# Kernel tuning notes

Measured on AMD Instinct MI355X. Metric: run time of the kernel, lower is better.

## Reference

```python
import jax, jax.numpy as jnp
import numpy as np

N, E, CIN, A, C, NB, B = 20000, 100000, 64, 32, 256, 4, 128
FD = C * NB  # fusion_dims = channels + c_growth*(n_blocks_out-1) with c_growth==channels
HID = 1024


def setup_inputs() -> dict:
    key = jax.random.key(0)
    ks = jax.random.split(key, 24)
    s = 0.05
    inp = {
        "x": jax.random.normal(ks[0], (N, CIN), jnp.float32),
        "edges": jax.random.randint(ks[1], (2, E), 0, N, jnp.int32),
        "edge_weights": jax.random.uniform(ks[2], (E,), jnp.float32),
        "edge_attrs": jax.random.normal(ks[3], (E, A), jnp.float32),
        "bbox_idx": jax.random.randint(ks[4], (N,), 0, B, jnp.int32),
        "num_boxes": B,
        # head GraphConv params: message MLP on [x_dst, x_src-x_dst, edge_attr]
        "W_msg0": jax.random.normal(ks[5], (2 * CIN + A, C), jnp.float32) * s,
        "b_msg0": jnp.zeros((C,), jnp.float32),
        "W_sup0": jax.random.normal(ks[6], (C + CIN, C), jnp.float32) * s,
        "b_sup0": jnp.zeros((C,), jnp.float32),
        # ResBlock params (n_blocks-1 blocks)
        "W_msg": jax.random.normal(ks[7], (NB - 1, 2 * C + A, C), jnp.float32) * s,
        "b_msg": jnp.zeros((NB - 1, C), jnp.float32),
        "W_sup": jax.random.normal(ks[8], (NB - 1, 2 * C, C), jnp.float32) * s,
        "b_sup": jnp.zeros((NB - 1, C), jnp.float32),
        # fusion MLPs [fusion_dims -> 1024]
        "W_fuse": jax.random.normal(ks[9], (FD, HID), jnp.float32) * s,
        "b_fuse": jnp.zeros((HID,), jnp.float32),
        "W_fuse_sup": jax.random.normal(ks[10], (FD, HID), jnp.float32) * s,
        "b_fuse_sup": jnp.zeros((HID,), jnp.float32),
    }
    return inp


def reference(x, edge_weights, edge_attrs, W_msg0, b_msg0, W_sup0, b_sup0,
              W_msg, b_msg, W_sup, b_sup, W_fuse, b_fuse, W_fuse_sup, b_fuse_sup,
              edges, bbox_idx, num_boxes):
    src, dst = edges[0], edges[1]
    n = x.shape[0]

    def gconv(f_in, Wm, bm):
        # per-edge message on [f_dst, f_src - f_dst, edge_attr], weighted sum-aggregate to dst
        h = jnp.concatenate([f_in[dst], f_in[src] - f_in[dst], edge_attrs], axis=1)
        m = jax.nn.relu(h @ Wm + bm) * edge_weights[:, None]
        return jax.ops.segment_sum(m, dst, num_segments=n)

    def super_node(f, x_node, Ws, bs):
        return jax.nn.relu(jnp.concatenate([f, x_node], axis=1) @ Ws + bs)

    # head GraphConv
    f = gconv(x, W_msg0, b_msg0)
    fs = super_node(f, x, W_sup0, b_sup0)
    feats, feats_super = [f], [fs]
    # ResBlocks: residual on node features, fresh super features
    for i in range(NB - 1):
        f = gconv(feats[-1], W_msg[i], b_msg[i]) + feats[-1]
        fs = super_node(f, feats_super[-1], W_sup[i], b_sup[i])
        feats.append(f)
        feats_super.append(fs)

    # n_blocks_out == n_blocks -> take all blocks
    feats_cat = jnp.concatenate(feats, axis=1)            # [N, FD]
    fusion = jax.nn.relu(feats_cat @ W_fuse + b_fuse)     # [N, 1024]
    out_feat = jnp.concatenate([fusion, feats_cat], axis=1)

    fs_cat = jnp.concatenate(feats_super, axis=1)         # [N, FD]
    sums = jax.ops.segment_sum(fs_cat, bbox_idx, num_segments=num_boxes)
    cnts = jax.ops.segment_sum(jnp.ones((n, 1), fs_cat.dtype), bbox_idx, num_segments=num_boxes)
    fs_mean = sums / jnp.maximum(cnts, 1.0)               # scatter(reduce='mean')
    fusion_sup = jax.nn.relu(fs_mean @ W_fuse_sup + b_fuse_sup)
    out_feat_super = jnp.concatenate([fusion_sup, fs_mean], axis=1)
    return out_feat, out_feat_super
```

## Files before the change

kernel.cpp:

```cpp
#include <hip/hip_runtime.h>

#define N_NODES 20000
#define N_EDGES 100000
#define CIN     64
#define A_DIM   32
#define CCH     256
#define NBOX    128
#define FD      1024
#define HID     1024
#define OUT_STRIDE 2048

typedef __attribute__((ext_vector_type(8))) short          short8;
typedef __attribute__((ext_vector_type(8))) unsigned short ushort8;
typedef __attribute__((ext_vector_type(4))) unsigned short ushort4v;
typedef __attribute__((ext_vector_type(4))) float          floatx4;

__device__ __forceinline__ unsigned short f2bf(float f) {
    unsigned int u = __float_as_uint(f);
    u += 0x7fff + ((u >> 16) & 1);
    return (unsigned short)(u >> 16);
}
__device__ __forceinline__ float bf2f(unsigned short h) {
    return __uint_as_float(((unsigned int)h) << 16);
}

__device__ __forceinline__ void glds16(const unsigned short* g, unsigned short* l) {
    __builtin_amdgcn_global_load_lds(
        (const __attribute__((address_space(1))) unsigned int*)g,
        (__attribute__((address_space(3))) unsigned int*)l,
        16, 0, 0);
}

struct GD {
    const unsigned short* src0b;
    const unsigned short* src1b;
    const unsigned short* Wt;
    const float* bias;
    const int* ridx0;
    float* outf;
    unsigned short* outb;
    int s0, o0, C0, s1, o1, do_relu, sof, oof, sob, oob, rmode, M, K, nbc;
};

__global__ __launch_bounds__(256) void mfma_dense(GD A, GD B, int n0)
{
    __shared__ __align__(16) unsigned short SM[2][4096];

    const int tid = threadIdx.x;
    const bool fa = (int)blockIdx.x < n0;

    const unsigned short* src0b = fa ? A.src0b : B.src0b;
    const unsigned short* src1b = fa ? A.src1b : B.src1b;
    const unsigned short* Wt    = fa ? A.Wt    : B.Wt;
    const float* bias           = fa ? A.bias  : B.bias;
    const int*   ridx0          = fa ? A.ridx0 : B.ridx0;
    float* outf                 = fa ? A.outf  : B.outf;
    unsigned short* outb        = fa ? A.outb  : B.outb;
    const int s0  = fa ? A.s0  : B.s0,  o0  = fa ? A.o0  : B.o0;
    const int C0  = fa ? A.C0  : B.C0;
    const int s1  = fa ? A.s1  : B.s1,  o1  = fa ? A.o1  : B.o1;
    const int do_relu = fa ? A.do_relu : B.do_relu;
    const int sof = fa ? A.sof : B.sof, oof = fa ? A.oof : B.oof;
    const int sob = fa ? A.sob : B.sob, oob = fa ? A.oob : B.oob;
    const int rmode = fa ? A.rmode : B.rmode;
    const int M   = fa ? A.M   : B.M;
    const int K   = fa ? A.K   : B.K;
    const int nbc = fa ? A.nbc : B.nbc;

    const int nwg = fa ? n0 : (int)gridDim.x - n0;
    const int lb  = (int)blockIdx.x - (fa ? 0 : n0);
    const int q8  = nwg >> 3, r8 = nwg & 7;
    const int xcd = lb & 7, boff = lb >> 3;
    const int bid = (xcd < r8 ? xcd * (q8 + 1)
                              : r8 * (q8 + 1) + (xcd - r8) * q8) + boff;

    const int rb   = bid / nbc, cb = bid % nbc;
    const int r0   = rb * 128, c0 = cb * 128;
    const int wave = tid >> 6, lane = tid & 63;
    const int quad = lane >> 4, l16 = lane & 15;
    const int wm   = (wave & 1) * 64, wn = (wave >> 1) * 64;

    int arow[2], grow[2], brow[2], kch[2];
    #pragma unroll
    for (int i = 0; i < 2; ++i) {
        const int g  = i * 256 + tid;
        const int rr = g >> 2;
        kch[i] = (g & 3) << 3;
        int gr2 = r0 + rr;
        if (gr2 >= M) gr2 = M - 1;
        grow[i] = gr2;
        arow[i] = ridx0 ? ridx0[gr2] : gr2;
        brow[i] = c0 + rr;
    }
    unsigned short* AsW = &SM[0][wave * 512];
    unsigned short* BsW = &SM[1][wave * 512];

    floatx4 acc[4][4];
    #pragma unroll
    for (int i = 0; i < 4; ++i)
        #pragma unroll
        for (int j = 0; j < 4; ++j) acc[i][j] = (floatx4){0.f, 0.f, 0.f, 0.f};

    for (int k0 = 0; k0 < K; k0 += 32) {
        #pragma unroll
        for (int i = 0; i < 2; ++i) {
            const int kk = k0 + kch[i];
            const unsigned short* ga = (kk < C0)
                ? src0b + (long)arow[i] * s0 + o0 + kk
                : src1b + (long)grow[i] * s1 + o1 + (kk - C0);
            glds16(ga, AsW + i * 2048);
            glds16(Wt + (long)brow[i] * K + k0 + kch[i], BsW + i * 2048);
        }
        __syncthreads();

        short8 af[4], bfr[4];
        #pragma unroll
        for (int mt = 0; mt < 4; ++mt)
            af[mt] = *(const short8*)(&SM[0][(wm + mt * 16 + l16) * 32 + quad * 8]);
        #pragma unroll
        for (int nt = 0; nt < 4; ++nt)
            bfr[nt] = *(const short8*)(&SM[1][(wn + nt * 16 + l16) * 32 + quad * 8]);
        #pragma unroll
        for (int mt = 0; mt < 4; ++mt)
            #pragma unroll
            for (int nt = 0; nt < 4; ++nt)
                acc[mt][nt] = __builtin_amdgcn_mfma_f32_16x16x32_bf16(
                    af[mt], bfr[nt], acc[mt][nt], 0, 0, 0);
        __syncthreads();
    }

    if (outf) {
        #pragma unroll
        for (int nt = 0; nt < 4; ++nt) {
            const int gc = c0 + wn + nt * 16 + l16;
            const float bv = bias ? bias[gc] : 0.f;
            #pragma unroll
            for (int mt = 0; mt < 4; ++mt) {
                #pragma unroll
                for (int reg = 0; reg < 4; ++reg) {
                    const int grr = r0 + wm + mt * 16 + quad * 4 + reg;
                    if (grr < M) {
                        float v = acc[mt][nt][reg] + bv;
                        if (do_relu) v = fmaxf(v, 0.f);
                        outf[(long)grr * sof + oof + gc] = v;
                    }
                }
            }
        }
    }
    if (outb) {
        unsigned short* Cs = &SM[0][0];
        #pragma unroll
        for (int p = 0; p < 2; ++p) {
            if (wm == p * 64) {
                #pragma unroll
                for (int nt = 0; nt < 4; ++nt) {
                    const int col = wn + nt * 16 + l16;
                    const float bv = bias ? bias[c0 + col] : 0.f;
                    #pragma unroll
                    for (int mt = 0; mt < 4; ++mt) {
                        #pragma unroll
                        for (int reg = 0; reg < 4; ++reg) {
                            float v = acc[mt][nt][reg] + bv;
                            if (do_relu) v = fmaxf(v, 0.f);
                            Cs[(mt * 16 + quad * 4 + reg) * 128 + col] = f2bf(v);
                        }
                    }
                }
            }
            __syncthreads();
            const int rl  = tid >> 2;
            const int cc0 = (tid & 3) << 3;
            const int grr2 = r0 + p * 64 + rl;
            if (grr2 < M) {
                const long rowbase = (rmode == 2)
                    ? ((long)(c0 >> 8) * ((long)N_EDGES * 256)
                       + (long)grr2 * 256 + (c0 & 255))
                    : ((long)grr2 * sob + oob + c0);
                #pragma unroll
                for (int j = 0; j < 4; ++j)
                    *(ushort8*)(outb + rowbase + cc0 + j * 32) =
                        *(const ushort8*)(&Cs[rl * 128 + cc0 + j * 32]);
            }
            __syncthreads();
        }
    }
}

__global__ __launch_bounds__(256) void agg_kernel(
    const unsigned short* __restrict__ pq,
    const int* __restrict__ rowptr,
    const int* __restrict__ ssrc,
    const float* __restrict__ sew,
    const unsigned short* __restrict__ Rb,
    const float* __restrict__ resid,
    const float* __restrict__ bias,
    float* __restrict__ out, int fofs, int rofs,
    unsigned short* __restrict__ nfbf, int nofs)
{
    const int wid  = (blockIdx.x * blockDim.x + threadIdx.x) >> 6;
    const int lane = threadIdx.x & 63;
    if (wid >= N_NODES) return;
    const int c = lane * 4;

    const ushort4v p4 = *(const ushort4v*)(pq + (long)wid * 512 + c);
    const float4 bb = *(const float4*)(bias + c);
    float pb[4] = {bf2f(p4[0]) + bb.x, bf2f(p4[1]) + bb.y,
                   bf2f(p4[2]) + bb.z, bf2f(p4[3]) + bb.w};
    float acc[4] = {0.f, 0.f, 0.f, 0.f};

    int s = rowptr[wid];
    const int sEnd = rowptr[wid + 1];

    ushort4v qA, rA, qB, rB;
    float wA = 0.f, wB = 0.f;
    if (s < sEnd) {
        const int n_ = ssrc[s];
        wA = sew[s];
        qA = *(const ushort4v*)(pq + (long)n_ * 512 + 256 + c);
        rA = *(const ushort4v*)(Rb + (long)s * 256 + c);
    }
    if (s + 1 < sEnd) {
        const int n_ = ssrc[s + 1];
        wB = sew[s + 1];
        qB = *(const ushort4v*)(pq + (long)n_ * 512 + 256 + c);
        rB = *(const ushort4v*)(Rb + (long)(s + 1) * 256 + c);
    }
    while (s + 1 < sEnd) {
        #pragma unroll
        for (int j = 0; j < 4; ++j)
            acc[j] += fmaxf(pb[j] + bf2f(qA[j]) + bf2f(rA[j]), 0.f) * wA;
        if (s + 2 < sEnd) {
            const int n_ = ssrc[s + 2];
            wA = sew[s + 2];
            qA = *(const ushort4v*)(pq + (long)n_ * 512 + 256 + c);
            rA = *(const ushort4v*)(Rb + (long)(s + 2) * 256 + c);
        }
        #pragma unroll
        for (int j = 0; j < 4; ++j)
            acc[j] += fmaxf(pb[j] + bf2f(qB[j]) + bf2f(rB[j]), 0.f) * wB;
        if (s + 3 < sEnd) {
            const int n_ = ssrc[s + 3];
            wB = sew[s + 3];
            qB = *(const ushort4v*)(pq + (long)n_ * 512 + 256 + c);
            rB = *(const ushort4v*)(Rb + (long)(s + 3) * 256 + c);
        }
        s += 2;
    }
    if (s < sEnd) {
        #pragma unroll
        for (int j = 0; j < 4; ++j)
            acc[j] += fmaxf(pb[j] + bf2f(qA[j]) + bf2f(rA[j]), 0.f) * wA;
    }
    if (rofs >= 0) {
        const float4 f4 = *(const float4*)(resid + (long)wid * OUT_STRIDE + rofs + c);
        acc[0] += f4.x; acc[1] += f4.y; acc[2] += f4.z; acc[3] += f4.w;
    }
    float4 o; o.x = acc[0]; o.y = acc[1]; o.z = acc[2]; o.w = acc[3];
    *(float4*)(out + (long)wid * OUT_STRIDE + fofs + c) = o;
    ushort4v hb = (ushort4v){f2bf(acc[0]), f2bf(acc[1]), f2bf(acc[2]), f2bf(acc[3])};
    *(ushort4v*)(nfbf + (long)wid * FD + nofs + c) = hb;
}

__device__ __forceinline__ void tr_block(const float* inp, unsigned short* outp,
                                         int K, int N, int bidx, int tid,
                                         float (*tile)[33])
{
    const int nbx = N >> 5;
    const int n0 = (bidx % nbx) << 5;
    const int k0 = (bidx / nbx) << 5;
    const int tx = tid & 31, ty = tid >> 5;
    #pragma unroll
    for (int r = 0; r < 4; ++r)
        tile[ty + r * 8][tx] = inp[(long)(k0 + ty + r * 8) * N + n0 + tx];
    __syncthreads();
    #pragma unroll
    for (int r = 0; r < 4; ++r)
        outp[(long)(n0 + ty + r * 8) * K + k0 + tx] = f2bf(tile[tx][ty + r * 8]);
}

#define PB_CVTX  1250
#define PB_CVTE  3125
#define PB_WPQ0  128
#define PB_WPQ3  384
#define PB_WTR   128
#define PB_TS0   80
#define PB_TS3   384
#define PB_TF    1024
#define PREP_BLOCKS (PB_CVTX+PB_CVTE+PB_WPQ0+PB_WPQ3+PB_WTR+PB_TS0+PB_TS3+PB_TF+PB_TF)

__global__ __launch_bounds__(256) void prep_all(
    const float* __restrict__ x, const float* __restrict__ ea,
    const float* __restrict__ W_msg0, const float* __restrict__ W_msg,
    const float* __restrict__ W_sup0, const float* __restrict__ W_sup,
    const float* __restrict__ W_fuse, const float* __restrict__ W_fsup,
    unsigned short* __restrict__ xb, unsigned short* __restrict__ eab,
    unsigned short* __restrict__ wpq0, unsigned short* __restrict__ wpq,
    unsigned short* __restrict__ wtr,
    unsigned short* __restrict__ wt_sup0, unsigned short* __restrict__ wt_sup,
    unsigned short* __restrict__ wt_fuse, unsigned short* __restrict__ wt_fsup)
{
    __shared__ float tile[32][33];
    const int tid = threadIdx.x;
    int b = blockIdx.x;

    if (b < PB_CVTX) {
        int i = b * 256 + tid;
        float4 v = ((const float4*)x)[i];
        ((ushort4v*)xb)[i] = (ushort4v){f2bf(v.x), f2bf(v.y), f2bf(v.z), f2bf(v.w)};
        return;
    }
    b -= PB_CVTX;
    if (b < PB_CVTE) {
        int i = b * 256 + tid;
        float4 v = ((const float4*)ea)[i];
        ((ushort4v*)eab)[i] = (ushort4v){f2bf(v.x), f2bf(v.y), f2bf(v.z), f2bf(v.w)};
        return;
    }
    b -= PB_CVTE;
    if (b < PB_WPQ0) {
        int i = b * 256 + tid;
        int nn = i >> 6, k = i & 63;
        float v = (nn < 256) ? (W_msg0[k * 256 + nn] - W_msg0[(64 + k) * 256 + nn])
                             : (W_msg0[(64 + k) * 256 + (nn - 256)]);
        wpq0[(long)nn * 64 + k] = f2bf(v);
        return;
    }
    b -= PB_WPQ0;
    if (b < PB_WPQ3) {
        const int slab = b / 128, bb = b % 128;
        const float* Wi = W_msg + (long)slab * 544 * 256;
        unsigned short* Wo = wpq + (long)slab * 512 * 256;
        const int n0 = (bb & 15) << 5;
        const int k0 = (bb >> 4) << 5;
        const int tx = tid & 31, ty = tid >> 5;
        #pragma unroll
        for (int r = 0; r < 4; ++r) {
            const int k = k0 + ty + r * 8;
            float v;
            if (n0 < 256)
                v = Wi[(long)k * 256 + n0 + tx] - Wi[(long)(256 + k) * 256 + n0 + tx];
            else
                v = Wi[(long)(256 + k) * 256 + (n0 - 256) + tx];
            tile[ty + r * 8][tx] = v;
        }
        __syncthreads();
        #pragma unroll
        for (int r = 0; r < 4; ++r)
            Wo[(long)(n0 + ty + r * 8) * 256 + k0 + tx] = f2bf(tile[tx][ty + r * 8]);
        return;
    }
    b -= PB_WPQ3;
    if (b < PB_WTR) {
        const int j = b >> 5;
        const float* Wi = (j == 0) ? (W_msg0 + 2 * CIN * 256)
                                   : (W_msg + (long)(j - 1) * 544 * 256 + 2 * CCH * 256);
        unsigned short* Wo = wtr + (long)j * 256 * 32;
        int i = (b & 31) * 256 + tid;
        int k = i >> 8, n = i & 255;
        Wo[(long)n * 32 + k] = f2bf(Wi[i]);
        return;
    }
    b -= PB_WTR;
    if (b < PB_TS0) { tr_block(W_sup0, wt_sup0, 320, 256, b, tid, tile); return; }
    b -= PB_TS0;
    if (b < PB_TS3) {
        const int slab = b / 128;
        tr_block(W_sup + (long)slab * 512 * 256, wt_sup + (long)slab * 256 * 512,
                 512, 256, b % 128, tid, tile);
        return;
    }
    b -= PB_TS3;
    if (b < PB_TF) { tr_block(W_fuse, wt_fuse, 1024, 1024, b, tid, tile); return; }
    b -= PB_TF;
    tr_block(W_fsup, wt_fsup, 1024, 1024, b, tid, tile);
}

__global__ void zero2(int* __restrict__ cnt, int* __restrict__ bcnt) {
    int i = blockIdx.x * blockDim.x + threadIdx.x;
    if (i < N_NODES + 1) cnt[i] = 0;
    else if (i - (N_NODES + 1) < 129) bcnt[i - (N_NODES + 1)] = 0;
}
__global__ void hist2(const int* __restrict__ dst, const int* __restrict__ bbox,
                      int* __restrict__ cnt, int* __restrict__ bcnt) {
    int i = blockIdx.x * blockDim.x + threadIdx.x;
    if (i < N_EDGES) atomicAdd(&cnt[dst[i]], 1);
    else if (i - N_EDGES < N_NODES) atomicAdd(&bcnt[bbox[i - N_EDGES]], 1);
}
__global__ __launch_bounds__(1024) void scan2(
    const int* __restrict__ cnt,  int* __restrict__ rowptr, int* __restrict__ ofs,
    const int* __restrict__ bcnt, int* __restrict__ bptr,   int* __restrict__ bofs)
{
    __shared__ int part[1024];
    const int tid = threadIdx.x;
    const int n = blockIdx.x == 0 ? N_NODES : NBOX;
    const int* c   = blockIdx.x == 0 ? cnt    : bcnt;
    int* rp        = blockIdx.x == 0 ? rowptr : bptr;
    int* op        = blockIdx.x == 0 ? ofs    : bofs;
    const int chunk = (n + 1023) >> 10;
    int s = 0;
    for (int j = 0; j < chunk; ++j) {
        int i = tid * chunk + j;
        if (i < n) s += c[i];
    }
    part[tid] = s; __syncthreads();
    for (int d = 1; d < 1024; d <<= 1) {
        int v = (tid >= d) ? part[tid - d] : 0;
        __syncthreads();
        part[tid] += v;
        __syncthreads();
    }
    int run = (tid > 0) ? part[tid - 1] : 0;
    for (int j = 0; j < chunk; ++j) {
        int i = tid * chunk + j;
        if (i < n) { rp[i] = run; op[i] = run; run += c[i]; }
    }
    if (tid == 1023) rp[n] = part[1023];
}
__global__ void scatter2(const int* __restrict__ src, const int* __restrict__ dst,
                         const float* __restrict__ ew, int* __restrict__ ofs,
                         int* __restrict__ ssrc, float* __restrict__ sew,
                         int* __restrict__ seid,
                         const int* __restrict__ bbox, int* __restrict__ bofs,
                         int* __restrict__ snode) {
    int i = blockIdx.x * blockDim.x + threadIdx.x;
    if (i < N_EDGES) {
        int pos = atomicAdd(&ofs[dst[i]], 1);
        ssrc[pos] = src[i];
        sew[pos]  = ew[i];
        seid[pos] = i;
    } else if (i - N_EDGES < N_NODES) {
        int j = i - N_EDGES;
        int pos = atomicAdd(&bofs[bbox[j]], 1);
        snode[pos] = j;
    }
}

__global__ __launch_bounds__(256) void box_mean_csr(
    const unsigned short* __restrict__ fsbf, const int* __restrict__ bptr,
    const int* __restrict__ snode, float* __restrict__ out_super,
    unsigned short* __restrict__ fsmeanb)
{
    const int b = blockIdx.x >> 2;
    const int c = ((blockIdx.x & 3) << 8) + threadIdx.x;
    const int s0 = bptr[b], s1 = bptr[b + 1];
    float sum = 0.f;
    int s = s0;
    unsigned short hn = 0;
    if (s < s1) hn = fsbf[(long)snode[s] * FD + c];
    while (s < s1) {
        const unsigned short h = hn;
        if (s + 1 < s1) hn = fsbf[(long)snode[s + 1] * FD + c];
        sum += bf2f(h);
        ++s;
    }
    const float mean = sum / fmaxf((float)(s1 - s0), 1.f);
    out_super[(long)b * OUT_STRIDE + HID + c] = mean;
    fsmeanb[(long)b * FD + c] = f2bf(mean);
}

extern "C" void kernel_launch(void* const* d_in, const int* in_sizes, int n_in,
                              void* d_out, int out_size, void* d_ws, size_t ws_size,
                              hipStream_t stream) {
    const float* x      = (const float*)d_in[0];
    const int*   edges  = (const int*)d_in[1];
    const float* ew     = (const float*)d_in[2];
    const float* ea     = (const float*)d_in[3];
    const int*   bbox   = (const int*)d_in[4];
    const float* W_msg0 = (const float*)d_in[6];
    const float* b_msg0 = (const float*)d_in[7];
    const float* W_sup0 = (const float*)d_in[8];
    const float* b_sup0 = (const float*)d_in[9];
    const float* W_msg  = (const float*)d_in[10];
    const float* b_msg  = (const float*)d_in[11];
    const float* W_sup  = (const float*)d_in[12];
    const float* b_sup  = (const float*)d_in[13];
    const float* W_fuse = (const float*)d_in[14];
    const float* b_fuse = (const float*)d_in[15];
    const float* W_fsup = (const float*)d_in[16];
    const float* b_fsup = (const float*)d_in[17];

    float* out       = (float*)d_out;
    float* out_super = out + (long)N_NODES * OUT_STRIDE;

    char* w = (char*)d_ws;
    auto alloc = [&](size_t bytes) { char* p = w; w += (bytes + 63) & ~63ULL; return p; };
    unsigned short* fsbf    = (unsigned short*)alloc((size_t)N_NODES * FD * 2);
    unsigned short* nfbf    = (unsigned short*)alloc((size_t)N_NODES * FD * 2);
    unsigned short* pq      = (unsigned short*)alloc((size_t)N_NODES * 512 * 2);
    unsigned short* xb      = (unsigned short*)alloc((size_t)N_NODES * CIN * 2);
    unsigned short* eab     = (unsigned short*)alloc((size_t)N_EDGES * A_DIM * 2);
    unsigned short* Rb4     = (unsigned short*)alloc((size_t)N_EDGES * 1024 * 2);
    unsigned short* wpq0    = (unsigned short*)alloc((size_t)512 * CIN * 2);
    unsigned short* wpq     = (unsigned short*)alloc((size_t)3 * 512 * CCH * 2);
    unsigned short* wtr     = (unsigned short*)alloc((size_t)4 * 256 * 32 * 2);
    unsigned short* wt_sup0 = (unsigned short*)alloc((size_t)256 * 320 * 2);
    unsigned short* wt_sup  = (unsigned short*)alloc((size_t)3 * 256 * 512 * 2);
    unsigned short* wt_fuse = (unsigned short*)alloc((size_t)1024 * 1024 * 2);
    unsigned short* wt_fsup = (unsigned short*)alloc((size_t)1024 * 1024 * 2);
    unsigned short* fsmeanb = (unsigned short*)alloc((size_t)NBOX * FD * 2);
    float* sew        = (float*)alloc((size_t)N_EDGES * 4);
    int* cnt          = (int*)alloc((size_t)(N_NODES + 1) * 4);
    int* rowptr       = (int*)alloc((size_t)(N_NODES + 1) * 4);
    int* ofs          = (int*)alloc((size_t)(N_NODES + 1) * 4);
    int* ssrc         = (int*)alloc((size_t)N_EDGES * 4);
    int* seid         = (int*)alloc((size_t)N_EDGES * 4);
    int* bcnt         = (int*)alloc(129 * 4);
    int* bptr         = (int*)alloc(129 * 4);
    int* bofs         = (int*)alloc(129 * 4);
    int* snode        = (int*)alloc((size_t)N_NODES * 4);

    const int* srcp = edges;
    const int* dstp = edges + N_EDGES;

    prep_all<<<PREP_BLOCKS, 256, 0, stream>>>(
        x, ea, W_msg0, W_msg, W_sup0, W_sup, W_fuse, W_fsup,
        xb, eab, wpq0, wpq, wtr, wt_sup0, wt_sup, wt_fuse, wt_fsup);

    zero2<<<(N_NODES + 130 + 255) / 256, 256, 0, stream>>>(cnt, bcnt);
    hist2<<<(N_EDGES + N_NODES + 255) / 256, 256, 0, stream>>>(dstp, bbox, cnt, bcnt);
    scan2<<<2, 1024, 0, stream>>>(cnt, rowptr, ofs, bcnt, bptr, bofs);
    scatter2<<<(N_EDGES + N_NODES + 255) / 256, 256, 0, stream>>>(
        srcp, dstp, ew, ofs, ssrc, sew, seid, bbox, bofs, snode);

    const int GRB = (N_NODES + 127) / 128;
    const int GEB = (N_EDGES + 127) / 128;
    const long RLS = (long)N_EDGES * 256;

    auto mk = [](const unsigned short* src0b, int s0, int o0, int C0,
                 const int* ridx0,
                 const unsigned short* src1b, int s1, int o1,
                 const unsigned short* Wt, const float* bias, int relu,
                 float* outf, int sof, int oof,
                 unsigned short* outb, int sob, int oob, int rmode,
                 int M, int K, int nbc) {
        GD g;
        g.src0b = src0b; g.s0 = s0; g.o0 = o0; g.C0 = C0;
        g.ridx0 = ridx0;
        g.src1b = src1b; g.s1 = s1; g.o1 = o1;
        g.Wt = Wt; g.bias = bias; g.do_relu = relu;
        g.outf = outf; g.sof = sof; g.oof = oof;
        g.outb = outb; g.sob = sob; g.oob = oob; g.rmode = rmode;
        g.M = M; g.K = K; g.nbc = nbc;
        return g;
    };

    GD gR   = mk(eab, A_DIM, 0, A_DIM, seid, nullptr, 0, 0, wtr, nullptr, 0,
                 nullptr, 0, 0, Rb4, 0, 0, 2, N_EDGES, A_DIM, 8);
    GD gPQh = mk(xb, CIN, 0, CIN, nullptr, nullptr, 0, 0, wpq0, nullptr, 0,
                 nullptr, 0, 0, pq, 512, 0, 0, N_NODES, CIN, 4);
    GD gS0  = mk(nfbf, FD, 0, CCH, nullptr, xb, CIN, 0, wt_sup0, b_sup0, 1,
                 nullptr, 0, 0, fsbf, FD, 0, 0, N_NODES, CCH + CIN, 2);
    GD gPQ[3], gS[3];
    for (int i = 0; i < 3; ++i) {
        gPQ[i] = mk(nfbf, FD, CCH * i, CCH, nullptr, nullptr, 0, 0,
                    wpq + (long)i * 512 * CCH, nullptr, 0,
                    nullptr, 0, 0, pq, 512, 0, 0, N_NODES, CCH, 4);
        gS[i]  = mk(nfbf, FD, CCH * (i + 1), CCH, nullptr, fsbf, FD, CCH * i,
                    wt_sup + (long)i * 256 * 512, b_sup + i * CCH, 1,
                    nullptr, 0, 0, fsbf, FD, CCH * (i + 1), 0, N_NODES, 2 * CCH, 2);
    }
    GD gFU  = mk(nfbf, FD, 0, FD, nullptr, nullptr, 0, 0, wt_fuse, b_fuse, 1,
                 out, OUT_STRIDE, 0, nullptr, 0, 0, 0, N_NODES, FD, 8);
    GD gFS  = mk(fsmeanb, FD, 0, FD, nullptr, nullptr, 0, 0, wt_fsup, b_fsup, 1,
                 out_super, OUT_STRIDE, 0, nullptr, 0, 0, 0, NBOX, FD, 8);

    const int AGRID = (N_NODES + 3) / 4;

    mfma_dense<<<GEB * 8 + GRB * 4, 256, 0, stream>>>(gR, gPQh, GEB * 8);

    agg_kernel<<<AGRID, 256, 0, stream>>>(pq, rowptr, ssrc, sew,
        Rb4, out, b_msg0, out, HID, -1, nfbf, 0);

    mfma_dense<<<GRB * 6, 256, 0, stream>>>(gS0, gPQ[0], GRB * 2);
    for (int i = 0; i < 3; ++i) {
        agg_kernel<<<AGRID, 256, 0, stream>>>(pq, rowptr, ssrc, sew,
            Rb4 + (long)(i + 1) * RLS, out, b_msg + i * CCH,
            out, HID + CCH * (i + 1), HID + CCH * i, nfbf, CCH * (i + 1));
        if (i < 2)
            mfma_dense<<<GRB * 6, 256, 0, stream>>>(gS[i], gPQ[i + 1], GRB * 2);
    }

    mfma_dense<<<GRB * 10, 256, 0, stream>>>(gS[2], gFU, GRB * 2);

    box_mean_csr<<<NBOX * 4, 256, 0, stream>>>(fsbf, bptr, snode, out_super, fsmeanb);
    mfma_dense<<<8, 256, 0, stream>>>(gFS, gFS, 8);
}
```

Measured before the change: 782.0 us.

## Double GEMM K-tile to 64 with XOR-swizzled LDS and zero-padded edge attrs

The MFMA GEMM now stages 64-wide K slices into a larger shared buffer, so it runs half as many loads and barriers per K. The LDS column chunk index is XOR-swizzled by row to avoid bank conflicts on the fragment reads. Because every K must now be a multiple of 64, the edge-attribute matrix and its transposed weight are zero-padded from 32 to 64 columns. That padding doubles the edge-feature GEMM's memory traffic and its wasted MFMA work.

```diff
diff --git a/kernel.cpp b/kernel.cpp
--- a/kernel.cpp
+++ b/kernel.cpp
@@ -44,7 +44,7 @@
 
 __global__ __launch_bounds__(256) void mfma_dense(GD A, GD B, int n0)
 {
-    __shared__ __align__(16) unsigned short SM[2][4096];
+    __shared__ __align__(16) unsigned short SM[2][8192];
 
     const int tid = threadIdx.x;
     const bool fa = (int)blockIdx.x < n0;
@@ -80,17 +80,15 @@
     const int quad = lane >> 4, l16 = lane & 15;
     const int wm   = (wave & 1) * 64, wn = (wave >> 1) * 64;
 
-    int arow[2], grow[2], brow[2], kch[2];
+    const int rr8  = tid >> 3;
+    const int kchS = (((tid & 7) ^ (rr8 & 7)) << 3);
+    int arowv[4], growv[4];
     #pragma unroll
-    for (int i = 0; i < 2; ++i) {
-        const int g  = i * 256 + tid;
-        const int rr = g >> 2;
-        kch[i] = (g & 3) << 3;
-        int gr2 = r0 + rr;
+    for (int i = 0; i < 4; ++i) {
+        int gr2 = r0 + i * 32 + rr8;
         if (gr2 >= M) gr2 = M - 1;
-        grow[i] = gr2;
-        arow[i] = ridx0 ? ridx0[gr2] : gr2;
-        brow[i] = c0 + rr;
+        growv[i] = gr2;
+        arowv[i] = ridx0 ? ridx0[gr2] : gr2;
     }
     unsigned short* AsW = &SM[0][wave * 512];
     unsigned short* BsW = &SM[1][wave * 512];
@@ -101,31 +99,40 @@
         #pragma unroll
         for (int j = 0; j < 4; ++j) acc[i][j] = (floatx4){0.f, 0.f, 0.f, 0.f};
 
-    for (int k0 = 0; k0 < K; k0 += 32) {
-        #pragma unroll
-        for (int i = 0; i < 2; ++i) {
-            const int kk = k0 + kch[i];
+    for (int k0 = 0; k0 < K; k0 += 64) {
+        const int kk = k0 + kchS;
+        #pragma unroll
+        for (int i = 0; i < 4; ++i) {
             const unsigned short* ga = (kk < C0)
-                ? src0b + (long)arow[i] * s0 + o0 + kk
-                : src1b + (long)grow[i] * s1 + o1 + (kk - C0);
+                ? src0b + (long)arowv[i] * s0 + o0 + kk
+                : src1b + (long)growv[i] * s1 + o1 + (kk - C0);
             glds16(ga, AsW + i * 2048);
-            glds16(Wt + (long)brow[i] * K + k0 + kch[i], BsW + i * 2048);
+            glds16(Wt + (long)(c0 + i * 32 + rr8) * K + kk, BsW + i * 2048);
         }
         __syncthreads();
 
-        short8 af[4], bfr[4];
-        #pragma unroll
-        for (int mt = 0; mt < 4; ++mt)
-            af[mt] = *(const short8*)(&SM[0][(wm + mt * 16 + l16) * 32 + quad * 8]);
-        #pragma unroll
-        for (int nt = 0; nt < 4; ++nt)
-            bfr[nt] = *(const short8*)(&SM[1][(wn + nt * 16 + l16) * 32 + quad * 8]);
-        #pragma unroll
-        for (int mt = 0; mt < 4; ++mt)
+        #pragma unroll
+        for (int ks = 0; ks < 2; ++ks) {
+            short8 af[4], bfr[4];
             #pragma unroll
-            for (int nt = 0; nt < 4; ++nt)
-                acc[mt][nt] = __builtin_amdgcn_mfma_f32_16x16x32_bf16(
-                    af[mt], bfr[nt], acc[mt][nt], 0, 0, 0);
+            for (int mt = 0; mt < 4; ++mt) {
+                const int r = wm + mt * 16 + l16;
+                af[mt] = *(const short8*)(
+                    &SM[0][r * 64 + ((((ks << 2) | quad) ^ (r & 7)) << 3)]);
+            }
+            #pragma unroll
+            for (int nt = 0; nt < 4; ++nt) {
+                const int r = wn + nt * 16 + l16;
+                bfr[nt] = *(const short8*)(
+                    &SM[1][r * 64 + ((((ks << 2) | quad) ^ (r & 7)) << 3)]);
+            }
+            #pragma unroll
+            for (int mt = 0; mt < 4; ++mt)
+                #pragma unroll
+                for (int nt = 0; nt < 4; ++nt)
+                    acc[mt][nt] = __builtin_amdgcn_mfma_f32_16x16x32_bf16(
+                        af[mt], bfr[nt], acc[mt][nt], 0, 0, 0);
+        }
         __syncthreads();
     }
 
@@ -283,7 +290,7 @@
 #define PB_CVTE  3125
 #define PB_WPQ0  128
 #define PB_WPQ3  384
-#define PB_WTR   128
+#define PB_WTR   256
 #define PB_TS0   80
 #define PB_TS3   384
 #define PB_TF    1024
@@ -312,9 +319,18 @@
     }
     b -= PB_CVTX;
     if (b < PB_CVTE) {
-        int i = b * 256 + tid;
-        float4 v = ((const float4*)ea)[i];
-        ((ushort4v*)eab)[i] = (ushort4v){f2bf(v.x), f2bf(v.y), f2bf(v.z), f2bf(v.w)};
+        int idx = b * 256 + tid;
+        int e = idx >> 3, col0 = (idx & 7) << 3;
+        ushort8 h;
+        if (col0 < 32) {
+            const float4* p = (const float4*)(ea + (long)e * 32 + col0);
+            float4 a = p[0], q = p[1];
+            h = (ushort8){f2bf(a.x), f2bf(a.y), f2bf(a.z), f2bf(a.w),
+                          f2bf(q.x), f2bf(q.y), f2bf(q.z), f2bf(q.w)};
+        } else {
+            h = (ushort8){0,0,0,0,0,0,0,0};
+        }
+        *(ushort8*)(eab + (long)idx * 8) = h;
         return;
     }
     b -= PB_CVTE;
@@ -352,13 +368,14 @@
     }
     b -= PB_WPQ3;
     if (b < PB_WTR) {
-        const int j = b >> 5;
+        const int j = b >> 6;
         const float* Wi = (j == 0) ? (W_msg0 + 2 * CIN * 256)
                                    : (W_msg + (long)(j - 1) * 544 * 256 + 2 * CCH * 256);
-        unsigned short* Wo = wtr + (long)j * 256 * 32;
-        int i = (b & 31) * 256 + tid;
-        int k = i >> 8, n = i & 255;
-        Wo[(long)n * 32 + k] = f2bf(Wi[i]);
+        unsigned short* Wo = wtr + (long)j * 256 * 64;
+        int i = (b & 63) * 256 + tid;
+        int n = i >> 6, k = i & 63;
+        Wo[(long)n * 64 + k] = (k < 32) ? f2bf(Wi[(long)k * 256 + n])
+                                        : (unsigned short)0;
         return;
     }
     b -= PB_WTR;
@@ -489,11 +506,11 @@
     unsigned short* nfbf    = (unsigned short*)alloc((size_t)N_NODES * FD * 2);
     unsigned short* pq      = (unsigned short*)alloc((size_t)N_NODES * 512 * 2);
     unsigned short* xb      = (unsigned short*)alloc((size_t)N_NODES * CIN * 2);
-    unsigned short* eab     = (unsigned short*)alloc((size_t)N_EDGES * A_DIM * 2);
+    unsigned short* eab     = (unsigned short*)alloc((size_t)N_EDGES * 64 * 2);
     unsigned short* Rb4     = (unsigned short*)alloc((size_t)N_EDGES * 1024 * 2);
     unsigned short* wpq0    = (unsigned short*)alloc((size_t)512 * CIN * 2);
     unsigned short* wpq     = (unsigned short*)alloc((size_t)3 * 512 * CCH * 2);
-    unsigned short* wtr     = (unsigned short*)alloc((size_t)4 * 256 * 32 * 2);
+    unsigned short* wtr     = (unsigned short*)alloc((size_t)4 * 256 * 64 * 2);
     unsigned short* wt_sup0 = (unsigned short*)alloc((size_t)256 * 320 * 2);
     unsigned short* wt_sup  = (unsigned short*)alloc((size_t)3 * 256 * 512 * 2);
     unsigned short* wt_fuse = (unsigned short*)alloc((size_t)1024 * 1024 * 2);
@@ -545,8 +562,8 @@
         return g;
     };
 
-    GD gR   = mk(eab, A_DIM, 0, A_DIM, seid, nullptr, 0, 0, wtr, nullptr, 0,
-                 nullptr, 0, 0, Rb4, 0, 0, 2, N_EDGES, A_DIM, 8);
+    GD gR   = mk(eab, 64, 0, 64, seid, nullptr, 0, 0, wtr, nullptr, 0,
+                 nullptr, 0, 0, Rb4, 0, 0, 2, N_EDGES, 64, 8);
     GD gPQh = mk(xb, CIN, 0, CIN, nullptr, nullptr, 0, 0, wpq0, nullptr, 0,
                  nullptr, 0, 0, pq, 512, 0, 0, N_NODES, CIN, 4);
     GD gS0  = mk(nfbf, FD, 0, CCH, nullptr, xb, CIN, 0, wt_sup0, b_sup0, 1,
```

New measurement: 806.2 us. 3.1% more time.
